# Performance work log

Hardware: AMD Instinct MI355X
Metric: run time of the kernel (lower is better)

The kernel has to match this reference:

```python
import jax, jax.numpy as jnp
import numpy as np

V, C, L, NH, NKV, HID, E, K, T, B = 32000, 1536, 2, 12, 4, 2048, 8, 2, 2048, 1
D = C // NH  # 128
NREP = NH // NKV
EPS = 1e-6

def _rms(x, w):
    return x * jax.lax.rsqrt(jnp.mean(x * x, axis=-1, keepdims=True) + EPS) * w


def setup_inputs() -> dict:
    key = jax.random.key(0)
    ks = jax.random.split(key, 14)
    s = 0.02
    inp = {
        "tokens": jax.random.randint(ks[0], (B, T), 0, V, dtype=jnp.int64),
        "emb": jax.random.normal(ks[1], (V, C), jnp.float32) * s,      # tied with output proj
        "pos": jax.random.normal(ks[2], (T, C), jnp.float32) * s,
        "wq": jax.random.normal(ks[3], (L, C, NH * D), jnp.float32) * s,
        "wk": jax.random.normal(ks[4], (L, C, NKV * D), jnp.float32) * s,
        "wv": jax.random.normal(ks[5], (L, C, NKV * D), jnp.float32) * s,
        "wo": jax.random.normal(ks[6], (L, C, C), jnp.float32) * s,
        "attn_norm_w": jnp.ones((L, C), jnp.float32),
        "ffn_norm_w": jnp.ones((L, C), jnp.float32),
        "gate": jax.random.normal(ks[7], (L, C, E), jnp.float32) * s,
        "ew1": jax.random.normal(ks[8], (L, E, C, HID), jnp.float32) * s,
        "ew2": jax.random.normal(ks[9], (L, E, HID, C), jnp.float32) * s,
        "ew3": jax.random.normal(ks[10], (L, E, C, HID), jnp.float32) * s,
        "final_norm_w": jnp.ones((C,), jnp.float32),
    }
    return inp


def _forward(tokens, emb, pos, wq, wk, wv, wo, attn_norm_w, ffn_norm_w, gate,
             ew1, ew2, ew3, final_norm_w):
    x = emb[tokens] + pos[None, :T]            # [B,T,C]; dropout=0 (eval)
    causal = jnp.tril(jnp.ones((T, T), bool))
    for l in range(L):
        # --- GQA attention ---
        h = _rms(x, attn_norm_w[l])
        q = (h @ wq[l]).reshape(B, T, NH, D).transpose(0, 2, 1, 3)     # [B,NH,T,D]
        k = (h @ wk[l]).reshape(B, T, NKV, D).transpose(0, 2, 1, 3)
        v = (h @ wv[l]).reshape(B, T, NKV, D).transpose(0, 2, 1, 3)
        k = jnp.repeat(k, NREP, axis=1)
        v = jnp.repeat(v, NREP, axis=1)
        scores = jnp.einsum("bhqd,bhkd->bhqk", q, k) / jnp.sqrt(jnp.float32(D))
        scores = jnp.where(causal, scores, jnp.finfo(scores.dtype).min)
        attn = jax.nn.softmax(scores, axis=-1)
        y = jnp.einsum("bhqk,bhkd->bhqd", attn, v)
        y = y.transpose(0, 2, 1, 3).reshape(B, T, C)
        x = x + y @ wo[l]
        # --- MoE FFN (top-k routed SwiGLU experts) ---
        xf = _rms(x, ffn_norm_w[l]).reshape(-1, C)                      # [N,C]
        probs = jax.nn.softmax(xf @ gate[l], axis=-1)                   # [N,E]
        topw, topi = jax.lax.top_k(probs, K)
        topw = topw / jnp.sum(topw, axis=-1, keepdims=True)
        dense_w = jnp.sum(jax.nn.one_hot(topi, E, dtype=xf.dtype) * topw[..., None], axis=1)  # [N,E]
        h1 = jnp.einsum("nc,ech->enh", xf, ew1[l])
        h3 = jnp.einsum("nc,ech->enh", xf, ew3[l])
        hh = jax.nn.silu(h1) * h3                                       # [E,N,HID]
        moe = jnp.einsum("ne,enh,ehc->nc", dense_w, hh, ew2[l])
        x = x + moe.reshape(B, T, C)
    x = _rms(x, final_norm_w)
    logits = x @ emb.T                                                   # tied output proj
    return logits


def reference(tokens, emb, pos, wq, wk, wv, wo, attn_norm_w, ffn_norm_w, gate,
              ew1, ew2, ew3, final_norm_w):
    return _forward(tokens, emb, pos, wq, wk, wv, wo, attn_norm_w, ffn_norm_w,
                    gate, ew1, ew2, ew3, final_norm_w)
```

## Files before the change

### kernel.cpp

```cpp
#include <hip/hip_runtime.h>
#include <hip/hip_bf16.h>
#include <math.h>

#define Tn   2048
#define Cn   1536
#define Vn   32000
#define NHn  12
#define NKVn 4
#define Dn   128
#define HIDn 2048
#define En   8
#define Kn   2
#define Ln   2
#define NREPn 3
#define EPSn 1e-6f
#define CHT  16
#define NCHn 4
#define QKVW 2560

using bf16 = __hip_bfloat16;
using bf16x8 = __attribute__((ext_vector_type(8))) short;
using f32x4v = __attribute__((ext_vector_type(4))) float;

__device__ __forceinline__ void split3(float v, short& h, short& m, short& lo) {
  bf16 b0 = __float2bfloat16(v);
  float r1 = v - __bfloat162float(b0);
  bf16 b1 = __float2bfloat16(r1);
  float r2 = r1 - __bfloat162float(b1);
  bf16 b2 = __float2bfloat16(r2);
  h = *reinterpret_cast<short*>(&b0);
  m = *reinterpret_cast<short*>(&b1);
  lo = *reinterpret_cast<short*>(&b2);
}
__device__ __forceinline__ float b2f(short s) {
  bf16 b = *reinterpret_cast<bf16*>(&s);
  return __bfloat162float(b);
}
__device__ __forceinline__ void gl_lds16(const void* g, void* l) {
  __builtin_amdgcn_global_load_lds((const __attribute__((address_space(1))) void*)g,
                                   (__attribute__((address_space(3))) void*)l, 16, 0, 0);
}

__global__ void embed_k(const int* __restrict__ tok, const float* __restrict__ emb,
                        const float* __restrict__ pos, float* __restrict__ x) {
  int n = blockIdx.x;
  int t = threadIdx.x;
  int id = tok[n];
  const float* er = emb + (size_t)id * Cn;
  const float* pr = pos + (size_t)n * Cn;
  float* xr = x + (size_t)n * Cn;
  for (int c = t; c < Cn; c += 256) xr[c] = er[c] + pr[c];
}

__global__ void rms3_k(const float* __restrict__ x, const float* __restrict__ w,
                       float* __restrict__ outf, short* __restrict__ dh,
                       short* __restrict__ dm, short* __restrict__ dl) {
  int n = blockIdx.x, t = threadIdx.x;
  const float* xr = x + (size_t)n * Cn;
  float v[6];
  float ss = 0.f;
#pragma unroll
  for (int i = 0; i < 6; i++) { v[i] = xr[t + i * 256]; ss += v[i] * v[i]; }
  for (int off = 32; off > 0; off >>= 1) ss += __shfl_down(ss, off, 64);
  __shared__ float red[4];
  __shared__ float rtot;
  int wave = t >> 6, lane = t & 63;
  if (lane == 0) red[wave] = ss;
  __syncthreads();
  if (t == 0) rtot = rsqrtf((red[0] + red[1] + red[2] + red[3]) / (float)Cn + EPSn);
  __syncthreads();
  float r = rtot;
#pragma unroll
  for (int i = 0; i < 6; i++) {
    int c = t + i * 256;
    float val = v[i] * r * w[c];
    size_t idx = (size_t)n * Cn + c;
    if (outf) outf[idx] = val;
    short h, m, lo;
    split3(val, h, m, lo);
    dh[idx] = h; dm[idx] = m; dl[idx] = lo;
  }
}

__global__ void rmsb_k(const float* __restrict__ x, const float* __restrict__ w,
                       float* __restrict__ outf, bf16* __restrict__ outb) {
  int n = blockIdx.x, t = threadIdx.x;
  const float* xr = x + (size_t)n * Cn;
  float v[6];
  float ss = 0.f;
#pragma unroll
  for (int i = 0; i < 6; i++) { v[i] = xr[t + i * 256]; ss += v[i] * v[i]; }
  for (int off = 32; off > 0; off >>= 1) ss += __shfl_down(ss, off, 64);
  __shared__ float red[4];
  __shared__ float rtot;
  int wave = t >> 6, lane = t & 63;
  if (lane == 0) red[wave] = ss;
  __syncthreads();
  if (t == 0) rtot = rsqrtf((red[0] + red[1] + red[2] + red[3]) / (float)Cn + EPSn);
  __syncthreads();
  float r = rtot;
#pragma unroll
  for (int i = 0; i < 6; i++) {
    int c = t + i * 256;
    float val = v[i] * r * w[c];
    size_t idx = (size_t)n * Cn + c;
    if (outf) outf[idx] = val;
    outb[idx] = __float2bfloat16(val);
  }
}

__global__ void f2b_k(const float* __restrict__ s, bf16* __restrict__ d, size_t n4) {
  size_t i = (size_t)blockIdx.x * 256 + threadIdx.x;
  size_t stride = (size_t)gridDim.x * 256;
  for (; i < n4; i += stride) {
    float4 v = ((const float4*)s)[i];
    d[i * 4 + 0] = __float2bfloat16(v.x);
    d[i * 4 + 1] = __float2bfloat16(v.y);
    d[i * 4 + 2] = __float2bfloat16(v.z);
    d[i * 4 + 3] = __float2bfloat16(v.w);
  }
}

__global__ void transp3_k(const float* __restrict__ src, short* __restrict__ dh,
                          short* __restrict__ dm, short* __restrict__ dl, int K, int N) {
  __shared__ __align__(16) float ls[32][33];
  size_t boff = (size_t)blockIdx.z * K * N;
  int k0 = blockIdx.x * 32, n0 = blockIdx.y * 32;
  int t = threadIdx.x;
  int kr = t >> 3, n4 = (t & 7) * 4;
  float4 vv = *(const float4*)&src[boff + (size_t)(k0 + kr) * N + n0 + n4];
  ls[kr][n4 + 0] = vv.x; ls[kr][n4 + 1] = vv.y; ls[kr][n4 + 2] = vv.z; ls[kr][n4 + 3] = vv.w;
  __syncthreads();
  int nr = t >> 3, k4 = (t & 7) * 4;
  size_t dbase = boff + (size_t)(n0 + nr) * K + k0 + k4;
#pragma unroll
  for (int u = 0; u < 4; u++) {
    short h, m, lo;
    split3(ls[k4 + u][nr], h, m, lo);
    dh[dbase + u] = h; dm[dbase + u] = m; dl[dbase + u] = lo;
  }
}

__global__ void transp_k(const float* __restrict__ src, bf16* __restrict__ dst, int K, int N) {
  __shared__ __align__(16) float ls[32][33];
  size_t boff = (size_t)blockIdx.z * K * N;
  int k0 = blockIdx.x * 32, n0 = blockIdx.y * 32;
  int t = threadIdx.x;
  int kr = t >> 3, n4 = (t & 7) * 4;
  float4 vv = *(const float4*)&src[boff + (size_t)(k0 + kr) * N + n0 + n4];
  ls[kr][n4 + 0] = vv.x; ls[kr][n4 + 1] = vv.y; ls[kr][n4 + 2] = vv.z; ls[kr][n4 + 3] = vv.w;
  __syncthreads();
  int nr = t >> 3, k4 = (t & 7) * 4;
  bf16* drow = dst + boff + (size_t)(n0 + nr) * K + k0 + k4;
#pragma unroll
  for (int u = 0; u < 4; u++) drow[u] = __float2bfloat16(ls[k4 + u][nr]);
}

__global__ void __launch_bounds__(256) gemm_btl(const bf16* __restrict__ A, const bf16* __restrict__ Bt,
                                                const float* res, float* Co, int M, int N, int K) {
  __shared__ __align__(16) bf16 As[128 * 32];
  __shared__ __align__(16) bf16 Bs[128 * 32];
  int t = threadIdx.x;
  int l = t & 63, w = t >> 6;
  int bm = blockIdx.x * 128, bn = blockIdx.y * 128;
  int wr = (w >> 1) * 64, wc = (w & 1) * 64;
  const f32x4v zero = {0.f, 0.f, 0.f, 0.f};
  f32x4v acc[4][4];
#pragma unroll
  for (int i = 0; i < 4; i++)
#pragma unroll
    for (int j = 0; j < 4; j++) acc[i][j] = zero;
  const bf16* ag0 = A + (size_t)(bm + (t >> 2)) * K + (t & 3) * 8;
  const bf16* ag1 = A + (size_t)(bm + 64 + (t >> 2)) * K + (t & 3) * 8;
  const bf16* bg0 = Bt + (size_t)(bn + (t >> 2)) * K + (t & 3) * 8;
  const bf16* bg1 = Bt + (size_t)(bn + 64 + (t >> 2)) * K + (t & 3) * 8;
  int rl = l & 15, ko = (l >> 4) * 8;
  for (int k0 = 0; k0 < K; k0 += 32) {
    gl_lds16(ag0 + k0, (char*)As + t * 16);
    gl_lds16(ag1 + k0, (char*)As + (256 + t) * 16);
    gl_lds16(bg0 + k0, (char*)Bs + t * 16);
    gl_lds16(bg1 + k0, (char*)Bs + (256 + t) * 16);
    __syncthreads();
    bf16x8 a[4], b[4];
#pragma unroll
    for (int i = 0; i < 4; i++) a[i] = *(const bf16x8*)(As + (wr + i * 16 + rl) * 32 + ko);
#pragma unroll
    for (int j = 0; j < 4; j++) b[j] = *(const bf16x8*)(Bs + (wc + j * 16 + rl) * 32 + ko);
#pragma unroll
    for (int i = 0; i < 4; i++)
#pragma unroll
      for (int j = 0; j < 4; j++)
        acc[i][j] = __builtin_amdgcn_mfma_f32_16x16x32_bf16(a[i], b[j], acc[i][j], 0, 0, 0);
    __syncthreads();
  }
#pragma unroll
  for (int i = 0; i < 4; i++) {
    int rbase = bm + wr + i * 16 + (l >> 4) * 4;
#pragma unroll
    for (int j = 0; j < 4; j++) {
      int col = bn + wc + j * 16 + (l & 15);
#pragma unroll
      for (int r = 0; r < 4; r++) {
        size_t idx = (size_t)(rbase + r) * N + col;
        float v = acc[i][j][r];
        if (res) v += res[idx];
        Co[idx] = v;
      }
    }
  }
}

__global__ void __launch_bounds__(256) gemm6(const bf16* __restrict__ AH, const bf16* __restrict__ AM,
                                             const bf16* __restrict__ AL,
                                             const bf16* __restrict__ BH, const bf16* __restrict__ BM,
                                             const bf16* __restrict__ BL,
                                             const float* res, float* __restrict__ Co,
                                             int M, int N, int K) {
  __shared__ __align__(16) bf16 sAH[128 * 32], sAM[128 * 32], sAL[128 * 32];
  __shared__ __align__(16) bf16 sBH[128 * 32], sBM[128 * 32], sBL[128 * 32];
  int t = threadIdx.x;
  int l = t & 63, w = t >> 6;
  int bm = blockIdx.x * 128, bn = blockIdx.y * 128;
  int wr = (w >> 1) * 64, wc = (w & 1) * 64;
  const f32x4v zero = {0.f, 0.f, 0.f, 0.f};
  f32x4v acc[4][4];
#pragma unroll
  for (int i = 0; i < 4; i++)
#pragma unroll
    for (int j = 0; j < 4; j++) acc[i][j] = zero;
  size_t a0 = (size_t)(bm + (t >> 2)) * K + (t & 3) * 8;
  size_t a1 = (size_t)(bm + 64 + (t >> 2)) * K + (t & 3) * 8;
  size_t b0 = (size_t)(bn + (t >> 2)) * K + (t & 3) * 8;
  size_t b1 = (size_t)(bn + 64 + (t >> 2)) * K + (t & 3) * 8;
  int rl = l & 15, ko = (l >> 4) * 8;
  for (int k0 = 0; k0 < K; k0 += 32) {
    gl_lds16(AH + a0 + k0, (char*)sAH + t * 16);
    gl_lds16(AH + a1 + k0, (char*)sAH + (256 + t) * 16);
    gl_lds16(AM + a0 + k0, (char*)sAM + t * 16);
    gl_lds16(AM + a1 + k0, (char*)sAM + (256 + t) * 16);
    gl_lds16(AL + a0 + k0, (char*)sAL + t * 16);
    gl_lds16(AL + a1 + k0, (char*)sAL + (256 + t) * 16);
    gl_lds16(BH + b0 + k0, (char*)sBH + t * 16);
    gl_lds16(BH + b1 + k0, (char*)sBH + (256 + t) * 16);
    gl_lds16(BM + b0 + k0, (char*)sBM + t * 16);
    gl_lds16(BM + b1 + k0, (char*)sBM + (256 + t) * 16);
    gl_lds16(BL + b0 + k0, (char*)sBL + t * 16);
    gl_lds16(BL + b1 + k0, (char*)sBL + (256 + t) * 16);
    __syncthreads();
    bf16x8 aH[4], aM[4], aL[4];
#pragma unroll
    for (int i = 0; i < 4; i++) {
      int ro = (wr + i * 16 + rl) * 32 + ko;
      aH[i] = *(const bf16x8*)(sAH + ro);
      aM[i] = *(const bf16x8*)(sAM + ro);
      aL[i] = *(const bf16x8*)(sAL + ro);
    }
#pragma unroll
    for (int j = 0; j < 4; j++) {
      int ro = (wc + j * 16 + rl) * 32 + ko;
      bf16x8 bh = *(const bf16x8*)(sBH + ro);
      bf16x8 bm_ = *(const bf16x8*)(sBM + ro);
      bf16x8 bl = *(const bf16x8*)(sBL + ro);
#pragma unroll
      for (int i = 0; i < 4; i++) {
        acc[i][j] = __builtin_amdgcn_mfma_f32_16x16x32_bf16(aL[i], bh, acc[i][j], 0, 0, 0);
        acc[i][j] = __builtin_amdgcn_mfma_f32_16x16x32_bf16(aH[i], bl, acc[i][j], 0, 0, 0);
        acc[i][j] = __builtin_amdgcn_mfma_f32_16x16x32_bf16(aM[i], bm_, acc[i][j], 0, 0, 0);
        acc[i][j] = __builtin_amdgcn_mfma_f32_16x16x32_bf16(aM[i], bh, acc[i][j], 0, 0, 0);
        acc[i][j] = __builtin_amdgcn_mfma_f32_16x16x32_bf16(aH[i], bm_, acc[i][j], 0, 0, 0);
        acc[i][j] = __builtin_amdgcn_mfma_f32_16x16x32_bf16(aH[i], bh, acc[i][j], 0, 0, 0);
      }
    }
    __syncthreads();
  }
#pragma unroll
  for (int i = 0; i < 4; i++) {
    int rbase = bm + wr + i * 16 + (l >> 4) * 4;
#pragma unroll
    for (int j = 0; j < 4; j++) {
      int col = bn + wc + j * 16 + (l & 15);
#pragma unroll
      for (int r = 0; r < 4; r++) {
        size_t idx = (size_t)(rbase + r) * N + col;
        float v = acc[i][j][r];
        if (res) v += res[idx];
        Co[idx] = v;
      }
    }
  }
}

__global__ void __launch_bounds__(256) mexp6(const bf16* __restrict__ AH, const bf16* __restrict__ AM,
                                             const bf16* __restrict__ AL,
                                             const bf16* __restrict__ BH, const bf16* __restrict__ BM,
                                             const bf16* __restrict__ BL,
                                             const int* __restrict__ perm, const int* __restrict__ cnt,
                                             int ebase,
                                             short* __restrict__ HH, short* __restrict__ HM,
                                             short* __restrict__ HL,
                                             float* __restrict__ Co, int K, int N, int mode) {
  int e = ebase + blockIdx.z;
  int nrows = cnt[e];
  int bm = blockIdx.x * 128;
  if (bm >= nrows) return;
  int bn = blockIdx.y * 128;
  size_t eoff = (size_t)blockIdx.z * K * N;
  __shared__ __align__(16) bf16 sAH[128 * 32], sAM[128 * 32], sAL[128 * 32];
  __shared__ __align__(16) bf16 sBH[128 * 32], sBM[128 * 32], sBL[128 * 32];
  __shared__ int prow[128];
  int t = threadIdx.x, l = t & 63, w = t >> 6;
  if (t < 128) {
    int i = bm + t;
    prow[t] = (i < nrows) ? perm[e * Tn + i] : -1;
  }
  __syncthreads();
  int wr = (w >> 1) * 64, wc = (w & 1) * 64;
  const f32x4v zero = {0.f, 0.f, 0.f, 0.f};
  f32x4v acc[4][4];
#pragma unroll
  for (int i = 0; i < 4; i++)
#pragma unroll
    for (int j = 0; j < 4; j++) acc[i][j] = zero;
  int p0 = prow[t >> 2], p1 = prow[64 + (t >> 2)];
  int g0r = (p0 >= 0) ? (mode == 2 ? p0 : (p0 >> 1)) : 0;
  int g1r = (p1 >= 0) ? (mode == 2 ? p1 : (p1 >> 1)) : 0;
  size_t a0 = (size_t)g0r * K + (t & 3) * 8;
  size_t a1 = (size_t)g1r * K + (t & 3) * 8;
  size_t b0 = eoff + (size_t)(bn + (t >> 2)) * K + (t & 3) * 8;
  size_t b1 = eoff + (size_t)(bn + 64 + (t >> 2)) * K + (t & 3) * 8;
  int rl = l & 15, ko = (l >> 4) * 8;
  for (int k0 = 0; k0 < K; k0 += 32) {
    gl_lds16(AH + a0 + k0, (char*)sAH + t * 16);
    gl_lds16(AH + a1 + k0, (char*)sAH + (256 + t) * 16);
    gl_lds16(AM + a0 + k0, (char*)sAM + t * 16);
    gl_lds16(AM + a1 + k0, (char*)sAM + (256 + t) * 16);
    gl_lds16(AL + a0 + k0, (char*)sAL + t * 16);
    gl_lds16(AL + a1 + k0, (char*)sAL + (256 + t) * 16);
    gl_lds16(BH + b0 + k0, (char*)sBH + t * 16);
    gl_lds16(BH + b1 + k0, (char*)sBH + (256 + t) * 16);
    gl_lds16(BM + b0 + k0, (char*)sBM + t * 16);
    gl_lds16(BM + b1 + k0, (char*)sBM + (256 + t) * 16);
    gl_lds16(BL + b0 + k0, (char*)sBL + t * 16);
    gl_lds16(BL + b1 + k0, (char*)sBL + (256 + t) * 16);
    __syncthreads();
    bf16x8 aH[4], aM[4], aL[4];
#pragma unroll
    for (int i = 0; i < 4; i++) {
      int ro = (wr + i * 16 + rl) * 32 + ko;
      aH[i] = *(const bf16x8*)(sAH + ro);
      aM[i] = *(const bf16x8*)(sAM + ro);
      aL[i] = *(const bf16x8*)(sAL + ro);
    }
#pragma unroll
    for (int j = 0; j < 4; j++) {
      int ro = (wc + j * 16 + rl) * 32 + ko;
      bf16x8 bh = *(const bf16x8*)(sBH + ro);
      bf16x8 bm_ = *(const bf16x8*)(sBM + ro);
      bf16x8 bl = *(const bf16x8*)(sBL + ro);
#pragma unroll
      for (int i = 0; i < 4; i++) {
        acc[i][j] = __builtin_amdgcn_mfma_f32_16x16x32_bf16(aL[i], bh, acc[i][j], 0, 0, 0);
        acc[i][j] = __builtin_amdgcn_mfma_f32_16x16x32_bf16(aH[i], bl, acc[i][j], 0, 0, 0);
        acc[i][j] = __builtin_amdgcn_mfma_f32_16x16x32_bf16(aM[i], bm_, acc[i][j], 0, 0, 0);
        acc[i][j] = __builtin_amdgcn_mfma_f32_16x16x32_bf16(aM[i], bh, acc[i][j], 0, 0, 0);
        acc[i][j] = __builtin_amdgcn_mfma_f32_16x16x32_bf16(aH[i], bm_, acc[i][j], 0, 0, 0);
        acc[i][j] = __builtin_amdgcn_mfma_f32_16x16x32_bf16(aH[i], bh, acc[i][j], 0, 0, 0);
      }
    }
    __syncthreads();
  }
#pragma unroll
  for (int i = 0; i < 4; i++) {
#pragma unroll
    for (int r = 0; r < 4; r++) {
      int lrow = wr + i * 16 + (l >> 4) * 4 + r;
      int p = prow[lrow];
      if (p < 0) continue;
#pragma unroll
      for (int j = 0; j < 4; j++) {
        int col = bn + wc + j * 16 + (l & 15);
        size_t idx = (size_t)p * N + col;
        float v = acc[i][j][r];
        if (mode == 0) {
          short h, m, lo;
          split3(v, h, m, lo);
          HH[idx] = h; HM[idx] = m; HL[idx] = lo;
        } else if (mode == 1) {
          float v1 = b2f(HH[idx]) + b2f(HM[idx]) + b2f(HL[idx]);
          float hh = (v1 / (1.f + expf(-v1))) * v;
          short h, m, lo;
          split3(hh, h, m, lo);
          HH[idx] = h; HM[idx] = m; HL[idx] = lo;
        } else {
          Co[idx] = v;
        }
      }
    }
  }
}

__global__ void __launch_bounds__(256) mexpBd(const bf16* __restrict__ A, const bf16* __restrict__ B1,
                                              const bf16* __restrict__ B3,
                                              const int* __restrict__ perm, const int* __restrict__ cnt,
                                              int ebase, bf16* __restrict__ HB, int K, int N) {
  int e = ebase + blockIdx.z;
  int nrows = cnt[e];
  int bm = blockIdx.x * 128;
  if (bm >= nrows) return;
  int bn = blockIdx.y * 128;
  size_t eoff = (size_t)blockIdx.z * K * N;
  __shared__ __align__(16) bf16 sA[128 * 32];
  __shared__ __align__(16) bf16 s1[128 * 32];
  __shared__ __align__(16) bf16 s3[128 * 32];
  __shared__ int prow[128];
  int t = threadIdx.x, l = t & 63, w = t >> 6;
  if (t < 128) {
    int i = bm + t;
    prow[t] = (i < nrows) ? perm[e * Tn + i] : -1;
  }
  __syncthreads();
  int wr = (w >> 1) * 64, wc = (w & 1) * 64;
  const f32x4v zero = {0.f, 0.f, 0.f, 0.f};
  f32x4v acc1[4][4], acc3[4][4];
#pragma unroll
  for (int i = 0; i < 4; i++)
#pragma unroll
    for (int j = 0; j < 4; j++) { acc1[i][j] = zero; acc3[i][j] = zero; }
  int p0 = prow[t >> 2], p1 = prow[64 + (t >> 2)];
  int g0r = (p0 >= 0) ? (p0 >> 1) : 0;
  int g1r = (p1 >= 0) ? (p1 >> 1) : 0;
  size_t a0 = (size_t)g0r * K + (t & 3) * 8;
  size_t a1 = (size_t)g1r * K + (t & 3) * 8;
  size_t b0 = eoff + (size_t)(bn + (t >> 2)) * K + (t & 3) * 8;
  size_t b1 = eoff + (size_t)(bn + 64 + (t >> 2)) * K + (t & 3) * 8;
  int rl = l & 15, ko = (l >> 4) * 8;
  for (int k0 = 0; k0 < K; k0 += 32) {
    gl_lds16(A + a0 + k0, (char*)sA + t * 16);
    gl_lds16(A + a1 + k0, (char*)sA + (256 + t) * 16);
    gl_lds16(B1 + b0 + k0, (char*)s1 + t * 16);
    gl_lds16(B1 + b1 + k0, (char*)s1 + (256 + t) * 16);
    gl_lds16(B3 + b0 + k0, (char*)s3 + t * 16);
    gl_lds16(B3 + b1 + k0, (char*)s3 + (256 + t) * 16);
    __syncthreads();
    bf16x8 a[4];
#pragma unroll
    for (int i = 0; i < 4; i++) a[i] = *(const bf16x8*)(sA + (wr + i * 16 + rl) * 32 + ko);
#pragma unroll
    for (int j = 0; j < 4; j++) {
      int ro = (wc + j * 16 + rl) * 32 + ko;
      bf16x8 b1v = *(const bf16x8*)(s1 + ro);
      bf16x8 b3v = *(const bf16x8*)(s3 + ro);
#pragma unroll
      for (int i = 0; i < 4; i++) {
        acc1[i][j] = __builtin_amdgcn_mfma_f32_16x16x32_bf16(a[i], b1v, acc1[i][j], 0, 0, 0);
        acc3[i][j] = __builtin_amdgcn_mfma_f32_16x16x32_bf16(a[i], b3v, acc3[i][j], 0, 0, 0);
      }
    }
    __syncthreads();
  }
#pragma unroll
  for (int i = 0; i < 4; i++) {
#pragma unroll
    for (int r = 0; r < 4; r++) {
      int lrow = wr + i * 16 + (l >> 4) * 4 + r;
      int p = prow[lrow];
      if (p < 0) continue;
#pragma unroll
      for (int j = 0; j < 4; j++) {
        int col = bn + wc + j * 16 + (l & 15);
        float h1 = acc1[i][j][r], h3 = acc3[i][j][r];
        HB[(size_t)p * N + col] = __float2bfloat16((h1 / (1.f + expf(-h1))) * h3);
      }
    }
  }
}

__global__ void __launch_bounds__(256) mexpB(const bf16* __restrict__ A, const bf16* __restrict__ B,
                                             const int* __restrict__ perm, const int* __restrict__ cnt,
                                             int ebase, float* __restrict__ Co, int K, int N) {
  int e = ebase + blockIdx.z;
  int nrows = cnt[e];
  int bm = blockIdx.x * 128;
  if (bm >= nrows) return;
  int bn = blockIdx.y * 128;
  size_t eoff = (size_t)blockIdx.z * K * N;
  __shared__ __align__(16) bf16 sA[128 * 32];
  __shared__ __align__(16) bf16 sB[128 * 32];
  __shared__ int prow[128];
  int t = threadIdx.x, l = t & 63, w = t >> 6;
  if (t < 128) {
    int i = bm + t;
    prow[t] = (i < nrows) ? perm[e * Tn + i] : -1;
  }
  __syncthreads();
  int wr = (w >> 1) * 64, wc = (w & 1) * 64;
  const f32x4v zero = {0.f, 0.f, 0.f, 0.f};
  f32x4v acc[4][4];
#pragma unroll
  for (int i = 0; i < 4; i++)
#pragma unroll
    for (int j = 0; j < 4; j++) acc[i][j] = zero;
  int p0 = prow[t >> 2], p1 = prow[64 + (t >> 2)];
  int g0r = (p0 >= 0) ? p0 : 0;
  int g1r = (p1 >= 0) ? p1 : 0;
  size_t a0 = (size_t)g0r * K + (t & 3) * 8;
  size_t a1 = (size_t)g1r * K + (t & 3) * 8;
  size_t b0 = eoff + (size_t)(bn + (t >> 2)) * K + (t & 3) * 8;
  size_t b1 = eoff + (size_t)(bn + 64 + (t >> 2)) * K + (t & 3) * 8;
  int rl = l & 15, ko = (l >> 4) * 8;
  for (int k0 = 0; k0 < K; k0 += 32) {
    gl_lds16(A + a0 + k0, (char*)sA + t * 16);
    gl_lds16(A + a1 + k0, (char*)sA + (256 + t) * 16);
    gl_lds16(B + b0 + k0, (char*)sB + t * 16);
    gl_lds16(B + b1 + k0, (char*)sB + (256 + t) * 16);
    __syncthreads();
    bf16x8 a[4], b[4];
#pragma unroll
    for (int i = 0; i < 4; i++) a[i] = *(const bf16x8*)(sA + (wr + i * 16 + rl) * 32 + ko);
#pragma unroll
    for (int j = 0; j < 4; j++) b[j] = *(const bf16x8*)(sB + (wc + j * 16 + rl) * 32 + ko);
#pragma unroll
    for (int i = 0; i < 4; i++)
#pragma unroll
      for (int j = 0; j < 4; j++)
        acc[i][j] = __builtin_amdgcn_mfma_f32_16x16x32_bf16(a[i], b[j], acc[i][j], 0, 0, 0);
    __syncthreads();
  }
#pragma unroll
  for (int i = 0; i < 4; i++) {
#pragma unroll
    for (int r = 0; r < 4; r++) {
      int lrow = wr + i * 16 + (l >> 4) * 4 + r;
      int p = prow[lrow];
      if (p < 0) continue;
#pragma unroll
      for (int j = 0; j < 4; j++) {
        int col = bn + wc + j * 16 + (l & 15);
        Co[(size_t)p * N + col] = acc[i][j][r];
      }
    }
  }
}

__global__ void __launch_bounds__(256) attn_part_k(const float* __restrict__ qkv,
                                                   float* __restrict__ po,
                                                   float* __restrict__ pm,
                                                   float* __restrict__ pl) {
  int qt = blockIdx.x;
  int head = blockIdx.y;
  int ch = blockIdx.z;
  int ntiles = qt + 1;
  int tA = ch * CHT;
  int t = threadIdx.x;
  int r = t >> 3, g = t & 7, d0 = g * 16;
  int q0 = qt * 32;
  int row = q0 + r;
  size_t pidx = ((size_t)head * Tn + row) * NCHn + ch;
  if (tA >= ntiles) {
    if (g == 0) { pm[pidx] = -1e30f; pl[pidx] = 0.f; }
    float* porow = po + pidx * Dn + d0;
#pragma unroll
    for (int j = 0; j < 16; j += 4) {
      float4 z = {0.f, 0.f, 0.f, 0.f};
      *(float4*)(porow + j) = z;
    }
    return;
  }
  int tB = tA + CHT < ntiles ? tA + CHT : ntiles;
  int kvh = head / NREPn;
  __shared__ __align__(16) float ks[32][Dn + 4];
  __shared__ __align__(16) float vs[32][Dn + 4];
  const float scale = 0.08838834764831845f;
  float qr[16];
  {
    const float* qrow = qkv + (size_t)row * QKVW + head * Dn + d0;
#pragma unroll
    for (int j = 0; j < 16; j += 4) {
      float4 u = *(const float4*)(qrow + j);
      qr[j] = u.x * scale; qr[j + 1] = u.y * scale;
      qr[j + 2] = u.z * scale; qr[j + 3] = u.w * scale;
    }
  }
  float o[16];
#pragma unroll
  for (int j = 0; j < 16; j++) o[j] = 0.f;
  float rowm = -1e30f, rowl = 0.f;

  for (int kt = tA; kt < tB; kt++) {
    int kv0 = kt * 32;
    for (int e = t; e < 32 * 32; e += 256) {
      int rr = e >> 5, c4 = (e & 31) * 4;
      size_t base = (size_t)(kv0 + rr) * QKVW + kvh * Dn + c4;
      *(float4*)&ks[rr][c4] = *(const float4*)(qkv + base + 1536);
      *(float4*)&vs[rr][c4] = *(const float4*)(qkv + base + 2048);
    }
    __syncthreads();
    float s[32];
#pragma unroll
    for (int kk = 0; kk < 32; kk++) {
      const float* krow = &ks[kk][d0];
      float p = 0.f;
#pragma unroll
      for (int j = 0; j < 16; j += 4) {
        float4 u = *(const float4*)(krow + j);
        p += qr[j] * u.x + qr[j + 1] * u.y + qr[j + 2] * u.z + qr[j + 3] * u.w;
      }
      p += __shfl_xor(p, 1);
      p += __shfl_xor(p, 2);
      p += __shfl_xor(p, 4);
      s[kk] = p;
    }
    if (kt == qt) {
#pragma unroll
      for (int kk = 0; kk < 32; kk++)
        if (kv0 + kk > row) s[kk] = -1e30f;
    }
    float mx = s[0];
#pragma unroll
    for (int kk = 1; kk < 32; kk++) mx = fmaxf(mx, s[kk]);
    float m_new = fmaxf(rowm, mx);
    float corr = expf(rowm - m_new);
    float sum = 0.f;
#pragma unroll
    for (int kk = 0; kk < 32; kk++) { s[kk] = expf(s[kk] - m_new); sum += s[kk]; }
    rowl = rowl * corr + sum;
    rowm = m_new;
#pragma unroll
    for (int j = 0; j < 16; j++) o[j] *= corr;
#pragma unroll
    for (int kk = 0; kk < 32; kk++) {
      float p = s[kk];
      const float* vrow = &vs[kk][d0];
#pragma unroll
      for (int j = 0; j < 16; j += 4) {
        float4 u = *(const float4*)(vrow + j);
        o[j] += p * u.x; o[j + 1] += p * u.y; o[j + 2] += p * u.z; o[j + 3] += p * u.w;
      }
    }
    __syncthreads();
  }
  if (g == 0) { pm[pidx] = rowm; pl[pidx] = rowl; }
  float* porow = po + pidx * Dn + d0;
#pragma unroll
  for (int j = 0; j < 16; j += 4) {
    float4 u;
    u.x = o[j]; u.y = o[j + 1]; u.z = o[j + 2]; u.w = o[j + 3];
    *(float4*)(porow + j) = u;
  }
}

__global__ void __launch_bounds__(256) attn_merge3_k(const float* __restrict__ po,
                                                     const float* __restrict__ pm,
                                                     const float* __restrict__ pl,
                                                     short* __restrict__ dh,
                                                     short* __restrict__ dm,
                                                     short* __restrict__ dl) {
  int qt = blockIdx.x;
  int head = blockIdx.y;
  int q0 = qt * 32;
  int t = threadIdx.x;
  int r = t >> 3, g = t & 7, d0 = g * 16;
  int row = q0 + r;
  size_t base = ((size_t)head * Tn + row) * NCHn;
  float M = -1e30f;
#pragma unroll
  for (int c = 0; c < NCHn; c++) M = fmaxf(M, pm[base + c]);
  float L = 0.f;
  float acc[16];
#pragma unroll
  for (int j = 0; j < 16; j++) acc[j] = 0.f;
#pragma unroll
  for (int c = 0; c < NCHn; c++) {
    float wgt = expf(pm[base + c] - M);
    L += pl[base + c] * wgt;
    const float* p = po + (base + c) * Dn + d0;
#pragma unroll
    for (int j = 0; j < 16; j += 4) {
      float4 u = *(const float4*)(p + j);
      acc[j] += wgt * u.x; acc[j + 1] += wgt * u.y;
      acc[j + 2] += wgt * u.z; acc[j + 3] += wgt * u.w;
    }
  }
  float inv = 1.f / L;
  size_t yidx = (size_t)row * Cn + head * Dn + d0;
#pragma unroll
  for (int j = 0; j < 16; j++) {
    short h, m, lo;
    split3(acc[j] * inv, h, m, lo);
    dh[yidx + j] = h; dm[yidx + j] = m; dl[yidx + j] = lo;
  }
}

__global__ void gate_k(const float* __restrict__ xf, const float* __restrict__ g,
                       float* __restrict__ gl) {
  int n = blockIdx.x, t = threadIdx.x;
  int e = t & 7, cs = t >> 3;
  const float* xr = xf + (size_t)n * Cn;
  float s = 0.f;
  for (int j = 0; j < Cn / 32; j++) {
    int c = cs + 32 * j;
    s += xr[c] * g[c * En + e];
  }
  __shared__ float red[256];
  red[t] = s;
  __syncthreads();
  if (t < 8) {
    float tot = 0.f;
    for (int j = 0; j < 32; j++) tot += red[t + 8 * j];
    gl[n * En + t] = tot;
  }
}

__global__ void route_k(const float* __restrict__ gl, float* __restrict__ topw,
                        int* __restrict__ cnt, int* __restrict__ perm) {
  int n = blockIdx.x * blockDim.x + threadIdx.x;
  if (n >= Tn) return;
  float p[En];
  float mx = -1e30f;
#pragma unroll
  for (int e = 0; e < En; e++) { p[e] = gl[n * En + e]; mx = fmaxf(mx, p[e]); }
  float s = 0.f;
#pragma unroll
  for (int e = 0; e < En; e++) { p[e] = expf(p[e] - mx); s += p[e]; }
  float invs = 1.f / s;
#pragma unroll
  for (int e = 0; e < En; e++) p[e] *= invs;
  int i0 = 0;
#pragma unroll
  for (int e = 1; e < En; e++) if (p[e] > p[i0]) i0 = e;
  int i1 = (i0 == 0) ? 1 : 0;
#pragma unroll
  for (int e = 0; e < En; e++) if (e != i0 && p[e] > p[i1]) i1 = e;
  float w0 = p[i0], w1 = p[i1], sw = w0 + w1;
  topw[2 * n]     = w0 / sw;
  topw[2 * n + 1] = w1 / sw;
  int pos0 = atomicAdd(&cnt[i0], 1);
  perm[i0 * Tn + pos0] = 2 * n;
  int pos1 = atomicAdd(&cnt[i1], 1);
  perm[i1 * Tn + pos1] = 2 * n + 1;
}

__global__ void combine_k(const float* __restrict__ pairout, const float* __restrict__ topw,
                          float* __restrict__ x) {
  int n = blockIdx.x, t = threadIdx.x;
  float w0 = topw[2 * n], w1 = topw[2 * n + 1];
  const float* p0 = pairout + (size_t)(2 * n) * Cn;
  const float* p1 = pairout + (size_t)(2 * n + 1) * Cn;
  float* xr = x + (size_t)n * Cn;
  for (int c = t; c < Cn; c += 256) xr[c] += w0 * p0[c] + w1 * p1[c];
}

extern "C" void kernel_launch(void* const* d_in, const int* in_sizes, int n_in,
                              void* d_out, int out_size, void* d_ws, size_t ws_size,
                              hipStream_t stream) {
  const int*   tokens = (const int*)d_in[0];
  const float* emb    = (const float*)d_in[1];
  const float* pos    = (const float*)d_in[2];
  const float* wq     = (const float*)d_in[3];
  const float* wk     = (const float*)d_in[4];
  const float* wv     = (const float*)d_in[5];
  const float* wo     = (const float*)d_in[6];
  const float* attn_nw= (const float*)d_in[7];
  const float* ffn_nw = (const float*)d_in[8];
  const float* gate   = (const float*)d_in[9];
  const float* ew1    = (const float*)d_in[10];
  const float* ew2    = (const float*)d_in[11];
  const float* ew3    = (const float*)d_in[12];
  const float* final_nw = (const float*)d_in[13];
  float* out = (float*)d_out;

  char* wsb = (char*)d_ws;
  const size_t NC = (size_t)Tn * Cn;
  size_t off = 0;
  auto alloc = [&](size_t bytes) -> size_t {
    off = (off + 255) & ~(size_t)255;
    size_t p = off;
    off += bytes;
    return p;
  };
  size_t o_x    = alloc(NC * 4);
  size_t o_h    = alloc(NC * 4);
  size_t o_gl   = alloc((size_t)Tn * En * 4);
  size_t o_topw = alloc((size_t)Tn * Kn * 4);
  size_t o_cnt  = alloc(64);
  size_t o_perm = alloc((size_t)En * Tn * 4);
  size_t wlvl   = (size_t)4 * Cn * HIDn * 2;
  size_t o_w    = alloc(3 * wlvl);
  size_t hs_lvl = NC * 2;
  size_t o_hs   = alloc(3 * hs_lvl);
  size_t o_qkv  = alloc((size_t)Tn * QKVW * 4);
  size_t o_yb   = alloc(NC * 4);
  size_t hb_lvl = (size_t)Tn * Kn * HIDn * 2;
  size_t o_hbs  = o_qkv;
  size_t end_hbs = o_hbs + 3 * hb_lvl;
  if (off < end_hbs) off = end_hbs;
  size_t o_pair = alloc(NC * 4);
  size_t o_po   = alloc((size_t)NHn * Tn * NCHn * Dn * 4);
  size_t o_pm   = alloc((size_t)NHn * Tn * NCHn * 4);
  size_t o_pl   = alloc((size_t)NHn * Tn * NCHn * 4);

  float* x       = (float*)(wsb + o_x);
  float* h       = (float*)(wsb + o_h);
  float* gl      = (float*)(wsb + o_gl);
  float* topw    = (float*)(wsb + o_topw);
  int*   cnt     = (int*)(wsb + o_cnt);
  int*   perm    = (int*)(wsb + o_perm);
  float* qkvb    = (float*)(wsb + o_qkv);
  float* pairout = (float*)(wsb + o_pair);
  bf16*  hb      = (bf16*)(wsb + o_pair);
  bf16*  embB    = (bf16*)(wsb + o_w);
  float* po      = (float*)(wsb + o_po);
  float* pm      = (float*)(wsb + o_pm);
  float* pl      = (float*)(wsb + o_pl);

  short* hs[3]; short* hbs[3]; short* ewT[3];
  for (int s = 0; s < 3; s++) {
    hs[s]  = (short*)(wsb + o_hs + (size_t)s * hs_lvl);
    hbs[s] = (short*)(wsb + o_hbs + (size_t)s * hb_lvl);
    ewT[s] = (short*)(wsb + o_w + (size_t)s * wlvl);
  }
  size_t qkvw_lvl = (size_t)QKVW * Cn * 2;
  size_t wo_lvl   = (size_t)Cn * Cn * 2;
  short* qkvT[3]; short* woT[3];
  for (int s = 0; s < 3; s++) {
    qkvT[s] = (short*)(wsb + o_w + (size_t)s * qkvw_lvl);
    woT[s]  = (short*)(wsb + o_w + 3 * qkvw_lvl + (size_t)s * wo_lvl);
  }
  bf16* ew1B = (bf16*)(wsb + o_w);
  bf16* ew3B = (bf16*)(wsb + o_w + wlvl);
  bf16* ew2B = (bf16*)(wsb + o_w);

  embed_k<<<Tn, 256, 0, stream>>>(tokens, emb, pos, x);
  for (int l = 0; l < Ln; l++) {
    const float* wq_l = wq + (size_t)l * Cn * (NHn * Dn);
    const float* wk_l = wk + (size_t)l * Cn * (NKVn * Dn);
    const float* wv_l = wv + (size_t)l * Cn * (NKVn * Dn);
    const float* wo_l = wo + (size_t)l * Cn * Cn;
    const float* g_l  = gate + (size_t)l * Cn * En;
    const float* e1_l = ew1 + (size_t)l * En * Cn * HIDn;
    const float* e2_l = ew2 + (size_t)l * En * HIDn * Cn;
    const float* e3_l = ew3 + (size_t)l * En * Cn * HIDn;

    transp3_k<<<dim3(Cn / 32, (NHn * Dn) / 32, 1), 256, 0, stream>>>(wq_l, qkvT[0], qkvT[1], qkvT[2], Cn, NHn * Dn);
    transp3_k<<<dim3(Cn / 32, (NKVn * Dn) / 32, 1), 256, 0, stream>>>(
        wk_l, qkvT[0] + (size_t)1536 * Cn, qkvT[1] + (size_t)1536 * Cn, qkvT[2] + (size_t)1536 * Cn, Cn, NKVn * Dn);
    transp3_k<<<dim3(Cn / 32, (NKVn * Dn) / 32, 1), 256, 0, stream>>>(
        wv_l, qkvT[0] + (size_t)2048 * Cn, qkvT[1] + (size_t)2048 * Cn, qkvT[2] + (size_t)2048 * Cn, Cn, NKVn * Dn);
    transp3_k<<<dim3(Cn / 32, Cn / 32, 1), 256, 0, stream>>>(wo_l, woT[0], woT[1], woT[2], Cn, Cn);
    rms3_k<<<Tn, 256, 0, stream>>>(x, attn_nw + (size_t)l * Cn, nullptr, hs[0], hs[1], hs[2]);
    gemm6<<<dim3(Tn / 128, QKVW / 128), 256, 0, stream>>>(
        (bf16*)hs[0], (bf16*)hs[1], (bf16*)hs[2], (bf16*)qkvT[0], (bf16*)qkvT[1], (bf16*)qkvT[2],
        nullptr, qkvb, Tn, QKVW, Cn);
    attn_part_k<<<dim3(Tn / 32, NHn, NCHn), 256, 0, stream>>>(qkvb, po, pm, pl);
    attn_merge3_k<<<dim3(Tn / 32, NHn), 256, 0, stream>>>(po, pm, pl, hs[0], hs[1], hs[2]);
    gemm6<<<dim3(Tn / 128, Cn / 128), 256, 0, stream>>>(
        (bf16*)hs[0], (bf16*)hs[1], (bf16*)hs[2], (bf16*)woT[0], (bf16*)woT[1], (bf16*)woT[2],
        x, x, Tn, Cn, Cn);

    if (l < Ln - 1) {
      rms3_k<<<Tn, 256, 0, stream>>>(x, ffn_nw + (size_t)l * Cn, h, hs[0], hs[1], hs[2]);
      gate_k<<<Tn, 256, 0, stream>>>(h, g_l, gl);
      hipMemsetAsync(cnt, 0, 64, stream);
      route_k<<<Tn / 256, 256, 0, stream>>>(gl, topw, cnt, perm);
      for (int half = 0; half < 2; half++) {
        size_t hoff = (size_t)half * 4 * Cn * HIDn;
        int eb = half * 4;
        transp3_k<<<dim3(Cn / 32, HIDn / 32, 4), 256, 0, stream>>>(e1_l + hoff, ewT[0], ewT[1], ewT[2], Cn, HIDn);
        mexp6<<<dim3(Tn / 128, HIDn / 128, 4), 256, 0, stream>>>(
            (bf16*)hs[0], (bf16*)hs[1], (bf16*)hs[2], (bf16*)ewT[0], (bf16*)ewT[1], (bf16*)ewT[2],
            perm, cnt, eb, hbs[0], hbs[1], hbs[2], nullptr, Cn, HIDn, 0);
        transp3_k<<<dim3(Cn / 32, HIDn / 32, 4), 256, 0, stream>>>(e3_l + hoff, ewT[0], ewT[1], ewT[2], Cn, HIDn);
        mexp6<<<dim3(Tn / 128, HIDn / 128, 4), 256, 0, stream>>>(
            (bf16*)hs[0], (bf16*)hs[1], (bf16*)hs[2], (bf16*)ewT[0], (bf16*)ewT[1], (bf16*)ewT[2],
            perm, cnt, eb, hbs[0], hbs[1], hbs[2], nullptr, Cn, HIDn, 1);
        transp3_k<<<dim3(HIDn / 32, Cn / 32, 4), 256, 0, stream>>>(e2_l + (size_t)half * 4 * HIDn * Cn, ewT[0], ewT[1], ewT[2], HIDn, Cn);
        mexp6<<<dim3(Tn / 128, Cn / 128, 4), 256, 0, stream>>>(
            (bf16*)hbs[0], (bf16*)hbs[1], (bf16*)hbs[2], (bf16*)ewT[0], (bf16*)ewT[1], (bf16*)ewT[2],
            perm, cnt, eb, hbs[0], hbs[1], hbs[2], pairout, HIDn, Cn, 2);
      }
    } else {
      bf16* hbf = (bf16*)hs[0];
      bf16* hbB = (bf16*)hbs[0];
      rmsb_k<<<Tn, 256, 0, stream>>>(x, ffn_nw + (size_t)l * Cn, h, hbf);
      gate_k<<<Tn, 256, 0, stream>>>(h, g_l, gl);
      hipMemsetAsync(cnt, 0, 64, stream);
      route_k<<<Tn / 256, 256, 0, stream>>>(gl, topw, cnt, perm);
      for (int half = 0; half < 2; half++) {
        size_t hoff = (size_t)half * 4 * Cn * HIDn;
        int eb = half * 4;
        transp_k<<<dim3(Cn / 32, HIDn / 32, 4), 256, 0, stream>>>(e1_l + hoff, ew1B, Cn, HIDn);
        transp_k<<<dim3(Cn / 32, HIDn / 32, 4), 256, 0, stream>>>(e3_l + hoff, ew3B, Cn, HIDn);
        mexpBd<<<dim3(Tn / 128, HIDn / 128, 4), 256, 0, stream>>>(
            hbf, ew1B, ew3B, perm, cnt, eb, hbB, Cn, HIDn);
        transp_k<<<dim3(HIDn / 32, Cn / 32, 4), 256, 0, stream>>>(e2_l + (size_t)half * 4 * HIDn * Cn, ew2B, HIDn, Cn);
        mexpB<<<dim3(Tn / 128, Cn / 128, 4), 256, 0, stream>>>(
            hbB, ew2B, perm, cnt, eb, pairout, HIDn, Cn);
      }
    }
    combine_k<<<Tn, 256, 0, stream>>>(pairout, topw, x);
  }
  rmsb_k<<<Tn, 256, 0, stream>>>(x, final_nw, nullptr, hb);
  f2b_k<<<2048, 256, 0, stream>>>(emb, embB, (size_t)Vn * Cn / 4);
  gemm_btl<<<dim3(Tn / 128, Vn / 128), 256, 0, stream>>>(hb, embB, nullptr, out, Tn, Vn, Cn);
}
```

Before: 4.997 ms.

## Compact split-K attention grid to only valid causal chunks with smaller chunk size

Replaces the fixed 4-chunk-per-query-tile attention grid (which launched many empty blocks that just wrote zeros) with a flattened grid that enumerates only the KV chunks each causal query tile actually needs. The chunk size drops from 16 to 8 KV tiles, so work per block is more balanced. The merge kernel reads a variable number of partials using a closed-form offset. This removes idle blocks and long tail blocks, at the cost of a serial index search per block and more partials to merge for late query tiles.

```diff
diff --git a/kernel.cpp b/kernel.cpp
--- a/kernel.cpp
+++ b/kernel.cpp
@@ -14,8 +14,8 @@
 #define Ln   2
 #define NREPn 3
 #define EPSn 1e-6f
-#define CHT  16
-#define NCHn 4
+#define CHT  8
+#define TOTCH 288
 #define QKVW 2560
 
 using bf16 = __hip_bfloat16;
@@ -546,27 +546,19 @@
                                                    float* __restrict__ po,
                                                    float* __restrict__ pm,
                                                    float* __restrict__ pl) {
-  int qt = blockIdx.x;
+  int c = blockIdx.x;
   int head = blockIdx.y;
-  int ch = blockIdx.z;
+  int qt = 0, accp = 0;
+  while (accp + (qt >> 3) + 1 <= c) { accp += (qt >> 3) + 1; qt++; }
+  int ch = c - accp;
   int ntiles = qt + 1;
   int tA = ch * CHT;
+  int tB = tA + CHT < ntiles ? tA + CHT : ntiles;
   int t = threadIdx.x;
   int r = t >> 3, g = t & 7, d0 = g * 16;
   int q0 = qt * 32;
   int row = q0 + r;
-  size_t pidx = ((size_t)head * Tn + row) * NCHn + ch;
-  if (tA >= ntiles) {
-    if (g == 0) { pm[pidx] = -1e30f; pl[pidx] = 0.f; }
-    float* porow = po + pidx * Dn + d0;
-#pragma unroll
-    for (int j = 0; j < 16; j += 4) {
-      float4 z = {0.f, 0.f, 0.f, 0.f};
-      *(float4*)(porow + j) = z;
-    }
-    return;
-  }
-  int tB = tA + CHT < ntiles ? tA + CHT : ntiles;
+  size_t pidx = ((size_t)head * TOTCH + c) * 32 + r;
   int kvh = head / NREPn;
   __shared__ __align__(16) float ks[32][Dn + 4];
   __shared__ __align__(16) float vs[32][Dn + 4];
@@ -661,19 +653,21 @@
   int t = threadIdx.x;
   int r = t >> 3, g = t & 7, d0 = g * 16;
   int row = q0 + r;
-  size_t base = ((size_t)head * Tn + row) * NCHn;
+  int f = qt >> 3, rr = qt & 7;
+  int P = qt + 4 * f * (f - 1) + rr * f;
+  int nch = f + 1;
+  size_t base = ((size_t)head * TOTCH + P) * 32 + r;
   float M = -1e30f;
-#pragma unroll
-  for (int c = 0; c < NCHn; c++) M = fmaxf(M, pm[base + c]);
+  for (int c = 0; c < nch; c++) M = fmaxf(M, pm[base + (size_t)c * 32]);
   float L = 0.f;
   float acc[16];
 #pragma unroll
   for (int j = 0; j < 16; j++) acc[j] = 0.f;
-#pragma unroll
-  for (int c = 0; c < NCHn; c++) {
-    float wgt = expf(pm[base + c] - M);
-    L += pl[base + c] * wgt;
-    const float* p = po + (base + c) * Dn + d0;
+  for (int c = 0; c < nch; c++) {
+    size_t idx = base + (size_t)c * 32;
+    float wgt = expf(pm[idx] - M);
+    L += pl[idx] * wgt;
+    const float* p = po + idx * Dn + d0;
 #pragma unroll
     for (int j = 0; j < 16; j += 4) {
       float4 u = *(const float4*)(p + j);
@@ -795,9 +789,9 @@
   size_t end_hbs = o_hbs + 3 * hb_lvl;
   if (off < end_hbs) off = end_hbs;
   size_t o_pair = alloc(NC * 4);
-  size_t o_po   = alloc((size_t)NHn * Tn * NCHn * Dn * 4);
-  size_t o_pm   = alloc((size_t)NHn * Tn * NCHn * 4);
-  size_t o_pl   = alloc((size_t)NHn * Tn * NCHn * 4);
+  size_t o_po   = alloc((size_t)NHn * TOTCH * 32 * Dn * 4);
+  size_t o_pm   = alloc((size_t)NHn * TOTCH * 32 * 4);
+  size_t o_pl   = alloc((size_t)NHn * TOTCH * 32 * 4);
 
   float* x       = (float*)(wsb + o_x);
   float* h       = (float*)(wsb + o_h);
@@ -851,7 +845,7 @@
     gemm6<<<dim3(Tn / 128, QKVW / 128), 256, 0, stream>>>(
         (bf16*)hs[0], (bf16*)hs[1], (bf16*)hs[2], (bf16*)qkvT[0], (bf16*)qkvT[1], (bf16*)qkvT[2],
         nullptr, qkvb, Tn, QKVW, Cn);
-    attn_part_k<<<dim3(Tn / 32, NHn, NCHn), 256, 0, stream>>>(qkvb, po, pm, pl);
+    attn_part_k<<<dim3(TOTCH, NHn), 256, 0, stream>>>(qkvb, po, pm, pl);
     attn_merge3_k<<<dim3(Tn / 32, NHn), 256, 0, stream>>>(po, pm, pl, hs[0], hs[1], hs[2]);
     gemm6<<<dim3(Tn / 128, Cn / 128), 256, 0, stream>>>(
         (bf16*)hs[0], (bf16*)hs[1], (bf16*)hs[2], (bf16*)woT[0], (bf16*)woT[1], (bf16*)woT[2],
```

Result: slower. 5.104 ms (+2.1%).
